# Kernel tuning notes

Measured on AMD Instinct MI355X. Metric: run time of the kernel, lower is better.

## Reference

```python
import jax, jax.numpy as jnp
import numpy as np

NC = 19
CH16, CH32 = 1024, 2048
B, H, W = 4, 64, 64
EPS = 1e-5


def bn_relu(x, gamma, beta):
    # Train-mode BatchNorm (batch statistics, as in torch default) + ReLU.
    axes = (0,) + tuple(range(2, x.ndim))  # reduce over batch + spatial
    mean = jnp.mean(x, axes, keepdims=True)
    var = jnp.var(x, axes, keepdims=True)
    shp = (1, -1) + (1,) * (x.ndim - 2)
    return jax.nn.relu((x - mean) * jax.lax.rsqrt(var + EPS) * gamma.reshape(shp) + beta.reshape(shp))


def setup_inputs() -> dict:
    key = jax.random.key(0)
    ks = jax.random.split(key, 10)
    def p(k, shape, fan):
        return jax.random.normal(k, shape, jnp.float32) / np.float32(np.sqrt(fan))
    ones = lambda c: jnp.ones((c,), jnp.float32)
    zeros = lambda c: jnp.zeros((c,), jnp.float32)
    return {
        "x": jax.random.normal(ks[0], (B, CH32, H, W), jnp.float32),
        "low_level_feature": jax.random.normal(ks[1], (B, CH16, H, W), jnp.float32),
        "W_L": p(ks[2], (NC, CH16), CH16), "b_L": zeros(NC),
        "W_X": p(ks[3], (512, CH32, 3, 3), CH32 * 9), "g_X": ones(512), "be_X": zeros(512),
        "W_phi": p(ks[4], (256, 512), 512), "g_phi": ones(256), "be_phi": zeros(256),
        "W_psi": p(ks[5], (256, 512), 512), "g_psi": ones(256), "be_psi": zeros(256),
        "W_delta": p(ks[6], (256, 512), 512), "g_delta": ones(256), "be_delta": zeros(256),
        "W_rho": p(ks[7], (512, 256), 256), "g_rho": ones(512), "be_rho": zeros(512),
        "W_g": p(ks[8], (512, 1024), 1024), "g_g": ones(512), "be_g": zeros(512),
        "W_out": p(ks[9], (NC, 512), 512), "b_out": zeros(NC),
    }


def reference(x, low_level_feature, W_L, b_L, W_X, g_X, be_X,
              W_phi, g_phi, be_phi, W_psi, g_psi, be_psi,
              W_delta, g_delta, be_delta, W_rho, g_rho, be_rho,
              W_g, g_g, be_g, W_out, b_out):
    b, _, h, w = x.shape
    # X = conv2d(2048->512, 3x3) + BN + ReLU
    Xf = jax.lax.conv_general_dilated(x, W_X, (1, 1), 'SAME',
                                      dimension_numbers=('NCHW', 'OIHW', 'NCHW'))
    Xf = bn_relu(Xf, g_X, be_X)                          # [b,512,h,w]
    # L = 1x1 conv (with bias) -> soft object regions
    L = jnp.einsum('bchw,nc->bnhw', low_level_feature, W_L) + b_L[None, :, None, None]
    l_flat = L.reshape(b, L.shape[1], -1)                # [b,nc,N]
    M = jax.nn.softmax(l_flat, axis=-1)                  # softmax over N
    X_flat = Xf.reshape(b, 512, -1)                      # [b,512,N]
    # f_k = (M @ X_flat^T)^T : object region features [b,512,nc]
    f_k = jnp.einsum('bkn,bcn->bck', M, X_flat)
    # phi/psi/delta: 1x1 conv1d + BN + ReLU
    query = bn_relu(jnp.einsum('oc,bck->bok', W_phi, f_k), g_phi, be_phi)      # [b,256,nc]
    key_ = bn_relu(jnp.einsum('oc,bcn->bon', W_psi, X_flat), g_psi, be_psi)    # [b,256,N]
    logit = jnp.einsum('bqk,bqn->bkn', query, key_)      # [b,nc,N]
    attn = jax.nn.softmax(logit, axis=1)                 # softmax over nc (dim 1)
    delta = bn_relu(jnp.einsum('oc,bck->bok', W_delta, f_k), g_delta, be_delta)  # [b,256,nc]
    attn_sum = jnp.einsum('bqk,bkn->bqn', delta, attn)   # [b,256,N]
    X_obj = bn_relu(jnp.einsum('oq,bqn->bon', W_rho, attn_sum), g_rho, be_rho)
    X_obj = X_obj.reshape(b, 512, h, w)
    concat = jnp.concatenate([Xf, X_obj], axis=1)        # [b,1024,h,w]
    X_bar = bn_relu(jnp.einsum('oc,bchw->bohw', W_g, concat), g_g, be_g)
    out = jnp.einsum('nc,bchw->bnhw', W_out, X_bar) + b_out[None, :, None, None]
    return out
```

## Files before the change

kernel.cpp:

```cpp
#include <hip/hip_runtime.h>
#include <hip/hip_bf16.h>
#include <cstdint>
#include <cstddef>

#define EPSV 1e-5f

typedef float f32x4 __attribute__((ext_vector_type(4)));
typedef _Float16 f16x8 __attribute__((ext_vector_type(8)));
typedef unsigned short ushortx8 __attribute__((ext_vector_type(8)));

__device__ __forceinline__ unsigned short f2h(float f) {
  _Float16 h = (_Float16)f;
  return *reinterpret_cast<unsigned short*>(&h);
}

__device__ __forceinline__ void gload16(const void* g, void* l) {
  __builtin_amdgcn_global_load_lds(
      (const __attribute__((address_space(1))) void*)g,
      (__attribute__((address_space(3))) void*)l, 16, 0, 0);
}

__global__ __launch_bounds__(256) void ocr_cvt_x(const float* __restrict__ x,
                                                 unsigned short* __restrict__ xT) {
  __shared__ float tile[64][65];
  int icb = blockIdx.x, h = blockIdx.y, b = blockIdx.z, t = threadIdx.x;
  const float* xp = x + ((size_t)b * 2048 + icb * 64) * 4096 + h * 64;
  #pragma unroll
  for (int r = 0; r < 16; ++r) {
    int icl = r * 4 + (t >> 6), w = t & 63;
    tile[icl][w] = xp[(size_t)icl * 4096 + w];
  }
  __syncthreads();
  #pragma unroll
  for (int it = 0; it < 2; ++it) {
    int w = it * 32 + (t >> 3), cb = (t & 7) * 8;
    ushortx8 o;
    #pragma unroll
    for (int j = 0; j < 8; ++j) o[j] = f2h(tile[cb + j][w]);
    *(ushortx8*)&xT[(((size_t)b * 66 + h + 1) * 66 + (w + 1)) * 2048 + icb * 64 + cb] = o;
  }
}

__global__ __launch_bounds__(256) void ocr_cvt_w(const float* __restrict__ Wx,
                                                 unsigned short* __restrict__ WT) {
  int oc = blockIdx.x >> 3;
  int ic = (blockIdx.x & 7) * 256 + threadIdx.x;
  const float* wp = Wx + ((size_t)oc * 2048 + ic) * 9;
  float v[9];
  #pragma unroll
  for (int t = 0; t < 9; ++t) v[t] = wp[t];
  #pragma unroll
  for (int t = 0; t < 9; ++t)
    WT[((size_t)t * 512 + oc) * 2048 + ic] = f2h(v[t]);
}

__global__ __launch_bounds__(256) void ocr_cvt_h2(const float* __restrict__ inA,
                                                  unsigned short* __restrict__ outA,
                                                  const float* __restrict__ inB,
                                                  unsigned short* __restrict__ outB) {
  int i = blockIdx.x * 256 + threadIdx.x;
  if (i < 131072) outA[i] = f2h(inA[i]);
  if (i < 524288) outB[i] = f2h(inB[i]);
}

__global__ __launch_bounds__(512, 2) void ocr_conv_mfma(const unsigned short* __restrict__ xT,
                                                        const unsigned short* __restrict__ WT,
                                                        float* __restrict__ Xf) {
  __shared__ __align__(16) char lds_raw[163840];
  float* red = (float*)lds_raw;

  const int t = threadIdx.x;
  const int wv = t >> 6, lane = t & 63;
  const int kg = lane >> 4, lc = lane & 15;
  const int ws = wv & 3, kh = wv >> 2;
  const int kh4 = kh * 4;

  const int hg  = blockIdx.x & 7;
  const int b   = (blockIdx.x >> 3) & 3;
  const int oct = blockIdx.x >> 5;
  const int oc0 = oct * 64, h0 = hg * 8;

  const char* gp[10]; int lo[10];
  #pragma unroll
  for (int i = 0; i < 10; ++i) {
    int c = wv * 10 + i;
    lo[i] = c * 1024;
    if (c < 38) {
      int cell = c * 64 + lane; if (cell > 2375) cell = 2375;
      int r = cell / 66, col = cell - r * 66; if (col > 63) col = 63;
      int tap = r >> 2, kgs = r & 3;
      gp[i] = (const char*)WT + (size_t)(((tap * 512 + oc0 + col) * 2048) + kgs * 8) * 2;
    } else {
      int c2 = c - 38;
      int cell = c2 * 64 + lane; if (cell > 2639) cell = 2639;
      int r = cell / 66, col = cell - r * 66;
      int row = r >> 2, kgs = r & 3;
      gp[i] = (const char*)xT + (size_t)((((b * 66 + h0 + row) * 66 + col) * 2048) + kgs * 8) * 2;
    }
  }

  f32x4 acc[4][8] = {};

  #pragma unroll
  for (int i = 0; i < 10; ++i) gload16(gp[i], lds_raw + lo[i]);
  asm volatile("s_waitcnt vmcnt(0)" ::: "memory");
  __builtin_amdgcn_s_barrier();

  int cur = 0;
  #pragma unroll 1
  for (int step = 0; step < 64; ++step) {
    if (step < 63) {
      unsigned adv = (unsigned)(step + 1) * 64u;
      int nxt = (cur ^ 1) * 81920;
      #pragma unroll
      for (int i = 0; i < 10; ++i) gload16(gp[i] + adv, lds_raw + nxt + lo[i]);
      asm volatile("s_waitcnt vmcnt(10)" ::: "memory");
    } else {
      asm volatile("s_waitcnt vmcnt(0)" ::: "memory");
    }
    __builtin_amdgcn_s_barrier();

    const short* As = (const short*)(lds_raw + cur * 81920);
    const short* Bs = (const short*)(lds_raw + cur * 81920 + 38912);
    __builtin_amdgcn_s_setprio(1);
    #pragma unroll
    for (int j = 0; j < 5; ++j) {
      const int tap = kh4 + j;
      const int dh = tap / 3, dw = tap - dh * 3;
      f16x8 av[4];
      #pragma unroll
      for (int mi = 0; mi < 4; ++mi)
        av[mi] = *(const f16x8*)&As[((tap * 4 + kg) * 66 + mi * 16 + lc) * 8];
      const int r0 = 2 * ws + dh;
      if ((tap != 4) || (kh == 0)) {
        #pragma unroll
        for (int nw = 0; nw < 4; ++nw) {
          f16x8 bv = *(const f16x8*)&Bs[((r0 * 4 + kg) * 66 + nw * 16 + lc + dw) * 8];
          #pragma unroll
          for (int mi = 0; mi < 4; ++mi)
            acc[mi][nw] = __builtin_amdgcn_mfma_f32_16x16x32_f16(av[mi], bv, acc[mi][nw], 0, 0, 0);
        }
      }
      if ((tap != 4) || (kh == 1)) {
        #pragma unroll
        for (int nw = 0; nw < 4; ++nw) {
          f16x8 bv = *(const f16x8*)&Bs[(((r0 + 1) * 4 + kg) * 66 + nw * 16 + lc + dw) * 8];
          #pragma unroll
          for (int mi = 0; mi < 4; ++mi)
            acc[mi][4 + nw] = __builtin_amdgcn_mfma_f32_16x16x32_f16(av[mi], bv, acc[mi][4 + nw], 0, 0, 0);
        }
      }
    }
    __builtin_amdgcn_s_setprio(0);
    asm volatile("s_waitcnt lgkmcnt(0)" ::: "memory");
    __builtin_amdgcn_sched_barrier(0);
    __builtin_amdgcn_s_barrier();
    cur ^= 1;
  }

  if (kh == 1) {
    #pragma unroll
    for (int mi = 0; mi < 4; ++mi)
      #pragma unroll
      for (int ni = 0; ni < 8; ++ni)
        *(f32x4*)&red[((ws * 32 + mi * 8 + ni) * 64 + lane) * 4] = acc[mi][ni];
  }
  __syncthreads();
  if (kh == 0) {
    #pragma unroll
    for (int mi = 0; mi < 4; ++mi) {
      #pragma unroll
      for (int ni = 0; ni < 8; ++ni) {
        f32x4 other = *(const f32x4*)&red[((ws * 32 + mi * 8 + ni) * 64 + lane) * 4];
        f32x4 s = acc[mi][ni] + other;
        int hh = ni >> 2, nw = ni & 3;
        int h = h0 + 2 * ws + hh;
        #pragma unroll
        for (int r = 0; r < 4; ++r) {
          int oc = oc0 + mi * 16 + (lane >> 4) * 4 + r;
          int w = nw * 16 + lc;
          Xf[(((size_t)b * 512 + oc) * 64 + h) * 64 + w] = s[r];
        }
      }
    }
  }
}

template<int K, int OT, int NT, int NWM, int NWN, int LDB>
__global__ __launch_bounds__(256) void ocr_gemm_h(const unsigned short* __restrict__ Ah,
                                                  const unsigned short* __restrict__ Bh,
                                                  float* __restrict__ Cm, int O) {
  static_assert(NT == 128, "NT fixed");
  constexpr int MI = OT / NWM / 16;
  constexpr int NI = NT / NWN / 16;
  constexpr int SA = OT + 2, SB = NT + 2;
  constexpr int ACELL = 4 * OT / 256;
  constexpr int ABUF = 4 * SA * 8;
  constexpr int BBUF = 4 * SB * 8;
  constexpr int NS = K / 32;
  constexpr int LPW = ACELL + 2;
  __shared__ __align__(16) short As_s[2 * ABUF];
  __shared__ __align__(16) short Bs_s[2 * BBUF];

  const int t = threadIdx.x;
  const int wv = t >> 6, lane = t & 63;
  const int kg = lane >> 4, lc = lane & 15;
  const int wm = wv / NWN, wn = wv % NWN;

  const int n0 = blockIdx.x * NT, o0 = blockIdx.y * OT, b = blockIdx.z;

  const char* aBase[ACELL]; int aLds[ACELL];
  #pragma unroll
  for (int r = 0; r < ACELL; ++r) {
    int flat0 = r * 256 + (t & 448);
    int flat  = flat0 + lane;
    int kgs = flat / OT, ol = flat % OT;
    aBase[r] = (const char*)(Ah + ((size_t)(o0 + ol)) * K + kgs * 8);
    aLds[r] = ((flat0 / OT) * SA + (flat0 % OT)) * 16;
  }
  const char* bBase[2]; int bLds[2];
  #pragma unroll
  for (int r = 0; r < 2; ++r) {
    int flat0 = r * 256 + (t & 448);
    int flat  = flat0 + lane;
    int kgs = flat >> 7, nl = flat & 127;
    bBase[r] = (const char*)(Bh + ((size_t)b * 4096 + n0 + nl) * LDB + kgs * 8);
    bLds[r] = ((flat0 >> 7) * SB + (flat0 & 127)) * 16;
  }

  f32x4 acc[MI][NI] = {};
  #pragma unroll
  for (int r = 0; r < ACELL; ++r) gload16(aBase[r], (char*)As_s + aLds[r]);
  #pragma unroll
  for (int r = 0; r < 2; ++r) gload16(bBase[r], (char*)Bs_s + bLds[r]);
  asm volatile("s_waitcnt vmcnt(0)" ::: "memory");
  __builtin_amdgcn_s_barrier();

  int cur = 0;
  #pragma unroll 1
  for (int step = 0; step < NS; ++step) {
    if (step + 1 < NS) {
      unsigned adv = (unsigned)(step + 1) * 64u;
      int nA = (cur ^ 1) * ABUF * 2, nB = (cur ^ 1) * BBUF * 2;
      #pragma unroll
      for (int r = 0; r < ACELL; ++r) gload16(aBase[r] + adv, (char*)As_s + nA + aLds[r]);
      #pragma unroll
      for (int r = 0; r < 2; ++r) gload16(bBase[r] + adv, (char*)Bs_s + nB + bLds[r]);
      if constexpr (LPW == 3) asm volatile("s_waitcnt vmcnt(3)" ::: "memory");
      else                    asm volatile("s_waitcnt vmcnt(4)" ::: "memory");
    } else {
      asm volatile("s_waitcnt vmcnt(0)" ::: "memory");
    }
    __builtin_amdgcn_s_barrier();

    const short* As = As_s + cur * ABUF;
    const short* Bsc = Bs_s + cur * BBUF;
    f16x8 av[MI], bv[NI];
    #pragma unroll
    for (int mi = 0; mi < MI; ++mi)
      av[mi] = *(const f16x8*)&As[(kg * SA + wm * (MI * 16) + mi * 16 + lc) * 8];
    #pragma unroll
    for (int ni = 0; ni < NI; ++ni)
      bv[ni] = *(const f16x8*)&Bsc[(kg * SB + wn * (NI * 16) + ni * 16 + lc) * 8];
    __builtin_amdgcn_s_setprio(1);
    #pragma unroll
    for (int mi = 0; mi < MI; ++mi)
      #pragma unroll
      for (int ni = 0; ni < NI; ++ni)
        acc[mi][ni] = __builtin_amdgcn_mfma_f32_16x16x32_f16(av[mi], bv[ni], acc[mi][ni], 0, 0, 0);
    __builtin_amdgcn_s_setprio(0);
    asm volatile("s_waitcnt lgkmcnt(0)" ::: "memory");
    __builtin_amdgcn_sched_barrier(0);
    __builtin_amdgcn_s_barrier();
    cur ^= 1;
  }
  #pragma unroll
  for (int mi = 0; mi < MI; ++mi) {
    #pragma unroll
    for (int ni = 0; ni < NI; ++ni) {
      int n = n0 + wn * (NI * 16) + ni * 16 + lc;
      #pragma unroll
      for (int r = 0; r < 4; ++r) {
        int oc = o0 + wm * (MI * 16) + mi * 16 + (lane >> 4) * 4 + r;
        Cm[((size_t)b * O + oc) * 4096 + n] = acc[mi][ni][r];
      }
    }
  }
}

__global__ __launch_bounds__(256) void ocr_t2h(const float* __restrict__ in,
                                               const float* __restrict__ scale,
                                               const float* __restrict__ shift,
                                               unsigned short* __restrict__ out,
                                               int C, int coff) {
  __shared__ float tile[64][65];
  int n0 = blockIdx.x * 64, c0 = blockIdx.y * 64, b = blockIdx.z;
  int t = threadIdx.x;
  #pragma unroll
  for (int r = 0; r < 16; ++r) {
    int c_l = r * 4 + (t >> 6), n_l = t & 63;
    tile[c_l][n_l] = in[((size_t)(b * C + c0 + c_l)) * 4096 + n0 + n_l];
  }
  __syncthreads();
  int n_l = t >> 2, cb = (t & 3) * 16;
  ushortx8 o0v, o1v;
  #pragma unroll
  for (int j = 0; j < 8; ++j) {
    int c = c0 + cb + j;
    o0v[j] = f2h(fmaxf(0.f, tile[cb + j][n_l] * scale[c] + shift[c]));
  }
  #pragma unroll
  for (int j = 0; j < 8; ++j) {
    int c = c0 + cb + 8 + j;
    o1v[j] = f2h(fmaxf(0.f, tile[cb + 8 + j][n_l] * scale[c] + shift[c]));
  }
  size_t base = ((size_t)b * 4096 + n0 + n_l) * 1024 + coff + c0 + cb;
  *(ushortx8*)&out[base] = o0v;
  *(ushortx8*)&out[base + 8] = o1v;
}

__global__ __launch_bounds__(256) void ocr_chan_stats(const float* __restrict__ buf,
                                                      const float* __restrict__ gamma,
                                                      const float* __restrict__ beta,
                                                      float* __restrict__ scale,
                                                      float* __restrict__ shift, int C) {
  int c = blockIdx.x, t = threadIdx.x;
  float s = 0.f, q = 0.f;
  for (int b = 0; b < 4; ++b) {
    const float* p = buf + ((size_t)b * C + c) * 4096;
    for (int i = t; i < 4096; i += 256) { float v = p[i]; s += v; q += v * v; }
  }
  __shared__ float ls[256], lq[256];
  ls[t] = s; lq[t] = q; __syncthreads();
  for (int off = 128; off > 0; off >>= 1) {
    if (t < off) { ls[t] += ls[t + off]; lq[t] += lq[t + off]; }
    __syncthreads();
  }
  if (t == 0) {
    float mean = ls[0] / 16384.f;
    float var  = lq[0] / 16384.f - mean * mean;
    float sc   = gamma[c] * rsqrtf(var + EPSV);
    scale[c] = sc; shift[c] = beta[c] - mean * sc;
  }
}

__global__ __launch_bounds__(256) void ocr_lproj(const float* __restrict__ llf,
                                                 const float* __restrict__ WL,
                                                 const float* __restrict__ bL,
                                                 float* __restrict__ L) {
  int h = blockIdx.x, b = blockIdx.y;
  int t = threadIdx.x, w = t & 63, csub = t >> 6;
  float acc[19];
  #pragma unroll
  for (int k = 0; k < 19; ++k) acc[k] = 0.f;
  const float* base = llf + ((size_t)b * 1024 + csub * 256) * 4096 + h * 64 + w;
  #pragma unroll 1
  for (int c4 = 0; c4 < 64; ++c4) {
    float lv[4];
    #pragma unroll
    for (int i = 0; i < 4; ++i) lv[i] = base[(size_t)(c4 + i * 64) * 4096];
    #pragma unroll
    for (int i = 0; i < 4; ++i) {
      const float* wl = &WL[csub * 256 + c4 + i * 64];
      #pragma unroll
      for (int k = 0; k < 19; ++k) acc[k] += wl[k * 1024] * lv[i];
    }
  }
  __shared__ float red[4][64][19];
  #pragma unroll
  for (int k = 0; k < 19; ++k) red[csub][w][k] = acc[k];
  __syncthreads();
  if (csub == 0) {
    #pragma unroll
    for (int k = 0; k < 19; ++k) {
      float s = red[0][w][k] + red[1][w][k] + red[2][w][k] + red[3][w][k] + bL[k];
      L[((size_t)b * 19 + k) * 4096 + h * 64 + w] = s;
    }
  }
}

__global__ __launch_bounds__(256) void ocr_softmax4096(float* __restrict__ buf) {
  int row = blockIdx.x, t = threadIdx.x;
  float* p = buf + (size_t)row * 4096;
  __shared__ float ls[256];
  float m = -1e30f;
  for (int i = t; i < 4096; i += 256) m = fmaxf(m, p[i]);
  ls[t] = m; __syncthreads();
  for (int off = 128; off > 0; off >>= 1) { if (t < off) ls[t] = fmaxf(ls[t], ls[t + off]); __syncthreads(); }
  m = ls[0]; __syncthreads();
  float s = 0.f;
  for (int i = t; i < 4096; i += 256) { float e = __expf(p[i] - m); p[i] = e; s += e; }
  ls[t] = s; __syncthreads();
  for (int off = 128; off > 0; off >>= 1) { if (t < off) ls[t] += ls[t + off]; __syncthreads(); }
  float inv = 1.f / ls[0];
  for (int i = t; i < 4096; i += 256) p[i] *= inv;
}

__global__ __launch_bounds__(256) void ocr_fk(const float* __restrict__ M,
                                              const float* __restrict__ Xf,
                                              const float* __restrict__ scale,
                                              const float* __restrict__ shift,
                                              float* __restrict__ fk) {
  int c = blockIdx.x, b = blockIdx.y, t = threadIdx.x;
  float acc[19];
  #pragma unroll
  for (int k = 0; k < 19; ++k) acc[k] = 0.f;
  const float* xp = Xf + ((size_t)b * 512 + c) * 4096;
  const float* mp = M + (size_t)b * 19 * 4096;
  float sc = scale[c], sh = shift[c];
  for (int n = t; n < 4096; n += 256) {
    float xv = fmaxf(0.f, xp[n] * sc + sh);
    #pragma unroll
    for (int k = 0; k < 19; ++k) acc[k] += mp[k * 4096 + n] * xv;
  }
  __shared__ float red[19 * 256];
  #pragma unroll
  for (int k = 0; k < 19; ++k) red[k * 256 + t] = acc[k];
  __syncthreads();
  for (int off = 128; off > 0; off >>= 1) {
    if (t < off) {
      #pragma unroll
      for (int k = 0; k < 19; ++k) red[k * 256 + t] += red[k * 256 + t + off];
    }
    __syncthreads();
  }
  if (t < 19) fk[((size_t)b * 512 + c) * 19 + t] = red[t * 256];
}

__global__ __launch_bounds__(256) void ocr_qd2(const float* __restrict__ Wphi,
                                               const float* __restrict__ Wdelta,
                                               const float* __restrict__ fk,
                                               float* __restrict__ qry,
                                               float* __restrict__ dlt) {
  int blk = blockIdx.x;
  const float* Wm = (blk < 76) ? Wphi : Wdelta;
  float* out = (blk < 76) ? qry : dlt;
  int tid = (blk < 76 ? blk : blk - 76) * 256 + threadIdx.x;
  if (tid >= 4 * 256 * 19) return;
  int k = tid % 19, o = (tid / 19) % 256, b = tid / (19 * 256);
  const float* fp = fk + (size_t)b * 512 * 19 + k;
  const float* wp = Wm + (size_t)o * 512;
  float acc = 0.f;
  for (int c = 0; c < 512; ++c) acc += wp[c] * fp[c * 19];
  out[tid] = acc;
}

__global__ __launch_bounds__(128) void ocr_bn76x2(float* __restrict__ qry,
                                                  float* __restrict__ dlt,
                                                  const float* __restrict__ g_phi,
                                                  const float* __restrict__ be_phi,
                                                  const float* __restrict__ g_delta,
                                                  const float* __restrict__ be_delta) {
  bool second = blockIdx.x >= 256;
  int o = blockIdx.x & 255, t = threadIdx.x;
  float* buf = second ? dlt : qry;
  const float* gamma = second ? g_delta : g_phi;
  const float* beta  = second ? be_delta : be_phi;
  bool act = t < 76;
  float v = 0.f;
  size_t idx = 0;
  if (act) {
    int b = t / 19, k = t % 19;
    idx = ((size_t)b * 256 + o) * 19 + k;
    v = buf[idx];
  }
  __shared__ float ls[128], lq[128];
  ls[t] = act ? v : 0.f; lq[t] = act ? v * v : 0.f; __syncthreads();
  for (int off = 64; off > 0; off >>= 1) { if (t < off) { ls[t] += ls[t + off]; lq[t] += lq[t + off]; } __syncthreads(); }
  __shared__ float s_sc, s_sh;
  if (t == 0) {
    float mean = ls[0] / 76.f;
    float var  = lq[0] / 76.f - mean * mean;
    float sc   = gamma[o] * rsqrtf(var + EPSV);
    s_sc = sc; s_sh = beta[o] - mean * sc;
  }
  __syncthreads();
  if (act) buf[idx] = fmaxf(0.f, v * s_sc + s_sh);
}

__global__ __launch_bounds__(256) void ocr_attn(const float* __restrict__ query,
                                                const float* __restrict__ key,
                                                const float* __restrict__ scale,
                                                const float* __restrict__ shift,
                                                float* __restrict__ attn) {
  int n0 = blockIdx.x * 64, b = blockIdx.y;
  int t = threadIdx.x, nl = t & 63, qsub = t >> 6;
  __shared__ float ql[256 * 19];
  for (int i = t; i < 256 * 19; i += 256) ql[i] = query[(size_t)b * 256 * 19 + i];
  __syncthreads();
  float acc[19];
  #pragma unroll
  for (int k = 0; k < 19; ++k) acc[k] = 0.f;
  const float* kp = key + ((size_t)b * 256 + qsub * 64) * 4096 + n0 + nl;
  #pragma unroll 1
  for (int q4 = 0; q4 < 64; q4 += 4) {
    float kv[4];
    #pragma unroll
    for (int i = 0; i < 4; ++i) kv[i] = kp[(size_t)(q4 + i) * 4096];
    #pragma unroll
    for (int i = 0; i < 4; ++i) {
      int ch = qsub * 64 + q4 + i;
      float kva = fmaxf(0.f, kv[i] * scale[ch] + shift[ch]);
      const float* qq = &ql[ch * 19];
      #pragma unroll
      for (int k = 0; k < 19; ++k) acc[k] += qq[k] * kva;
    }
  }
  __shared__ float red[4][64][19];
  #pragma unroll
  for (int k = 0; k < 19; ++k) red[qsub][nl][k] = acc[k];
  __syncthreads();
  if (qsub == 0) {
    float v[19]; float m = -1e30f;
    #pragma unroll
    for (int k = 0; k < 19; ++k) {
      v[k] = red[0][nl][k] + red[1][nl][k] + red[2][nl][k] + red[3][nl][k];
      m = fmaxf(m, v[k]);
    }
    float s = 0.f;
    #pragma unroll
    for (int k = 0; k < 19; ++k) { v[k] = __expf(v[k] - m); s += v[k]; }
    float inv = 1.f / s;
    #pragma unroll
    for (int k = 0; k < 19; ++k)
      attn[((size_t)b * 19 + k) * 4096 + n0 + nl] = v[k] * inv;
  }
}

__global__ __launch_bounds__(256) void ocr_wd(const float* __restrict__ Wrho,
                                              const float* __restrict__ dlt,
                                              float* __restrict__ Wd) {
  int tid = blockIdx.x * 256 + threadIdx.x;
  if (tid >= 4 * 512 * 19) return;
  int k = tid % 19, o = (tid / 19) % 512, b = tid / (19 * 512);
  const float* dp = dlt + (size_t)b * 256 * 19 + k;
  const float* wp = Wrho + (size_t)o * 256;
  float acc = 0.f;
  for (int q = 0; q < 256; ++q) acc += wp[q] * dp[q * 19];
  Wd[tid] = acc;
}

__global__ __launch_bounds__(256) void ocr_xobj_stats(const float* __restrict__ Wd,
                                                      const float* __restrict__ attn,
                                                      const float* __restrict__ gamma,
                                                      const float* __restrict__ beta,
                                                      float* __restrict__ scale,
                                                      float* __restrict__ shift) {
  int o = blockIdx.x, t = threadIdx.x;
  float s = 0.f, q = 0.f;
  for (int b = 0; b < 4; ++b) {
    float wd[19];
    #pragma unroll
    for (int k = 0; k < 19; ++k) wd[k] = Wd[((size_t)b * 512 + o) * 19 + k];
    for (int n = t; n < 4096; n += 256) {
      float v = 0.f;
      #pragma unroll
      for (int k = 0; k < 19; ++k) v += wd[k] * attn[((size_t)b * 19 + k) * 4096 + n];
      s += v; q += v * v;
    }
  }
  __shared__ float ls[256], lq[256];
  ls[t] = s; lq[t] = q; __syncthreads();
  for (int off = 128; off > 0; off >>= 1) {
    if (t < off) { ls[t] += ls[t + off]; lq[t] += lq[t + off]; }
    __syncthreads();
  }
  if (t == 0) {
    float mean = ls[0] / 16384.f;
    float var  = lq[0] / 16384.f - mean * mean;
    float sc   = gamma[o] * rsqrtf(var + EPSV);
    scale[o] = sc; shift[o] = beta[o] - mean * sc;
  }
}

__global__ __launch_bounds__(512) void ocr_xobj_apply(const float* __restrict__ Wd,
                                                      const float* __restrict__ attn,
                                                      const float* __restrict__ scale,
                                                      const float* __restrict__ shift,
                                                      unsigned short* __restrict__ ch) {
  __shared__ float al[19][256];
  int n0 = blockIdx.x * 256, b = blockIdx.y, o = threadIdx.x;
  for (int idx = o; idx < 19 * 256; idx += 512) {
    int k = idx >> 8, nl = idx & 255;
    al[k][nl] = attn[((size_t)b * 19 + k) * 4096 + n0 + nl];
  }
  float wd[19];
  #pragma unroll
  for (int k = 0; k < 19; ++k) wd[k] = Wd[((size_t)b * 512 + o) * 19 + k];
  float sc = scale[o], sh = shift[o];
  __syncthreads();
  #pragma unroll 1
  for (int nl = 0; nl < 256; ++nl) {
    float v = 0.f;
    #pragma unroll
    for (int k = 0; k < 19; ++k) v += wd[k] * al[k][nl];
    v = fmaxf(0.f, v * sc + sh);
    ch[((size_t)b * 4096 + n0 + nl) * 1024 + 512 + o] = f2h(v);
  }
}

__global__ __launch_bounds__(256) void ocr_out(const float* __restrict__ Wout,
                                               const float* __restrict__ bout,
                                               const float* __restrict__ Xbar,
                                               const float* __restrict__ scale,
                                               const float* __restrict__ shift,
                                               float* __restrict__ out) {
  int n0 = blockIdx.x * 64, b = blockIdx.y;
  int t = threadIdx.x, nl = t & 63, csub = t >> 6;
  float acc[19];
  #pragma unroll
  for (int k = 0; k < 19; ++k) acc[k] = 0.f;
  const float* base = Xbar + ((size_t)b * 512 + csub * 128) * 4096 + n0 + nl;
  #pragma unroll 1
  for (int c4 = 0; c4 < 128; c4 += 4) {
    float xv[4];
    #pragma unroll
    for (int i = 0; i < 4; ++i) xv[i] = base[(size_t)(c4 + i) * 4096];
    #pragma unroll
    for (int i = 0; i < 4; ++i) {
      int chn = csub * 128 + c4 + i;
      float a = fmaxf(0.f, xv[i] * scale[chn] + shift[chn]);
      #pragma unroll
      for (int k = 0; k < 19; ++k) acc[k] += Wout[k * 512 + chn] * a;
    }
  }
  __shared__ float red[4][64][19];
  #pragma unroll
  for (int k = 0; k < 19; ++k) red[csub][nl][k] = acc[k];
  __syncthreads();
  if (csub == 0) {
    #pragma unroll
    for (int k = 0; k < 19; ++k) {
      float s = red[0][nl][k] + red[1][nl][k] + red[2][nl][k] + red[3][nl][k] + bout[k];
      out[((size_t)b * 19 + k) * 4096 + n0 + nl] = s;
    }
  }
}

extern "C" void kernel_launch(void* const* d_in, const int* in_sizes, int n_in,
                              void* d_out, int out_size, void* d_ws, size_t ws_size,
                              hipStream_t stream) {
  const float* x    = (const float*)d_in[0];
  const float* llf  = (const float*)d_in[1];
  const float* W_L  = (const float*)d_in[2];
  const float* b_L  = (const float*)d_in[3];
  const float* W_X  = (const float*)d_in[4];
  const float* g_X  = (const float*)d_in[5];
  const float* be_X = (const float*)d_in[6];
  const float* W_phi = (const float*)d_in[7];
  const float* g_phi = (const float*)d_in[8];
  const float* be_phi = (const float*)d_in[9];
  const float* W_psi = (const float*)d_in[10];
  const float* g_psi = (const float*)d_in[11];
  const float* be_psi = (const float*)d_in[12];
  const float* W_delta = (const float*)d_in[13];
  const float* g_delta = (const float*)d_in[14];
  const float* be_delta = (const float*)d_in[15];
  const float* W_rho = (const float*)d_in[16];
  const float* g_rho = (const float*)d_in[17];
  const float* be_rho = (const float*)d_in[18];
  const float* W_g  = (const float*)d_in[19];
  const float* g_g  = (const float*)d_in[20];
  const float* be_g = (const float*)d_in[21];
  const float* W_out = (const float*)d_in[22];
  const float* b_out = (const float*)d_in[23];

  float* ws = (float*)d_ws;
  float* Xf = ws;
  float* U  = ws + 8388608;
  unsigned short* xT = (unsigned short*)U;
  unsigned short* WT = (unsigned short*)(U + 17842176);
  unsigned short* concat_h = (unsigned short*)U;
  float* key  = U + 8388608;
  float* Xbar = U + 12582912;
  float* SM   = U + 22560768;
  float* M     = SM;
  float* attnb = SM + 311296;
  float* fk    = SM + 622592;
  float* qry   = SM + 661504;
  float* dlt   = SM + 680960;
  float* Wd    = SM + 700416;
  float* st    = SM + 739328;
  unsigned short* Wpsi_h = (unsigned short*)(SM + 743424);
  unsigned short* Wg_h   = (unsigned short*)(SM + 808960);
  float* scX = st,        *shX = st + 512;
  float* scP = st + 1024, *shP = st + 1280;
  float* scR = st + 1536, *shR = st + 2048;
  float* scG = st + 2560, *shG = st + 3072;

  hipMemsetAsync(xT, 0, (size_t)35684352 * sizeof(unsigned short), stream);
  ocr_cvt_x<<<dim3(32, 64, 4), 256, 0, stream>>>(x, xT);
  ocr_cvt_w<<<dim3(4096), 256, 0, stream>>>(W_X, WT);
  ocr_cvt_h2<<<dim3(2048), 256, 0, stream>>>(W_psi, Wpsi_h, W_g, Wg_h);

  ocr_conv_mfma<<<dim3(256), 512, 0, stream>>>(xT, WT, Xf);

  ocr_chan_stats<<<dim3(512), 256, 0, stream>>>(Xf, g_X, be_X, scX, shX, 512);
  ocr_t2h<<<dim3(64, 8, 4), 256, 0, stream>>>(Xf, scX, shX, concat_h, 512, 0);
  ocr_lproj<<<dim3(64, 4), 256, 0, stream>>>(llf, W_L, b_L, M);
  ocr_softmax4096<<<dim3(76), 256, 0, stream>>>(M);
  ocr_fk<<<dim3(512, 4), 256, 0, stream>>>(M, Xf, scX, shX, fk);
  ocr_qd2<<<dim3(152), 256, 0, stream>>>(W_phi, W_delta, fk, qry, dlt);
  ocr_bn76x2<<<dim3(512), 128, 0, stream>>>(qry, dlt, g_phi, be_phi, g_delta, be_delta);
  ocr_gemm_h<512, 64, 128, 2, 2, 1024><<<dim3(32, 4, 4), 256, 0, stream>>>(Wpsi_h, concat_h, key, 256);
  ocr_chan_stats<<<dim3(256), 256, 0, stream>>>(key, g_psi, be_psi, scP, shP, 256);
  ocr_attn<<<dim3(64, 4), 256, 0, stream>>>(qry, key, scP, shP, attnb);
  ocr_wd<<<dim3(152), 256, 0, stream>>>(W_rho, dlt, Wd);
  ocr_xobj_stats<<<dim3(512), 256, 0, stream>>>(Wd, attnb, g_rho, be_rho, scR, shR);
  ocr_xobj_apply<<<dim3(16, 4), 512, 0, stream>>>(Wd, attnb, scR, shR, concat_h);
  ocr_gemm_h<1024, 128, 128, 2, 2, 1024><<<dim3(32, 4, 4), 256, 0, stream>>>(Wg_h, concat_h, Xbar, 512);
  ocr_chan_stats<<<dim3(512), 256, 0, stream>>>(Xbar, g_g, be_g, scG, shG, 512);
  ocr_out<<<dim3(64, 4), 256, 0, stream>>>(W_out, b_out, Xbar, scG, shG, (float*)d_out);
}
```

Before: 822.9 us.

## Double conv block to 1024 threads with one output row per wave

Grows the 3x3 conv MFMA kernel from 8 to 16 waves per block. Each wave now computes a single output row, so its accumulator set is halved and it issues half as many global-to-LDS loads. The centre tap is split across the two K-halves by output column halves instead of by row. The hand-tuned vmcnt waits, priority hints and scheduling barriers are replaced with plain __syncthreads, which costs fine-grained load/compute overlap. The launch-bounds hint of (1024, 4) may force a tight register budget and cause spills.

```diff
diff --git a/kernel.cpp b/kernel.cpp
--- a/kernel.cpp
+++ b/kernel.cpp
@@ -63,27 +63,26 @@
   if (i < 524288) outB[i] = f2h(inB[i]);
 }
 
-__global__ __launch_bounds__(512, 2) void ocr_conv_mfma(const unsigned short* __restrict__ xT,
-                                                        const unsigned short* __restrict__ WT,
-                                                        float* __restrict__ Xf) {
+__global__ __launch_bounds__(1024, 4) void ocr_conv_mfma(const unsigned short* __restrict__ xT,
+                                                         const unsigned short* __restrict__ WT,
+                                                         float* __restrict__ Xf) {
   __shared__ __align__(16) char lds_raw[163840];
   float* red = (float*)lds_raw;
 
   const int t = threadIdx.x;
   const int wv = t >> 6, lane = t & 63;
   const int kg = lane >> 4, lc = lane & 15;
-  const int ws = wv & 3, kh = wv >> 2;
-  const int kh4 = kh * 4;
+  const int ws = wv & 7, kh = wv >> 3;
 
   const int hg  = blockIdx.x & 7;
   const int b   = (blockIdx.x >> 3) & 3;
   const int oct = blockIdx.x >> 5;
   const int oc0 = oct * 64, h0 = hg * 8;
 
-  const char* gp[10]; int lo[10];
-  #pragma unroll
-  for (int i = 0; i < 10; ++i) {
-    int c = wv * 10 + i;
+  const char* gp[5]; int lo[5];
+  #pragma unroll
+  for (int i = 0; i < 5; ++i) {
+    int c = wv * 5 + i;
     lo[i] = c * 1024;
     if (c < 38) {
       int cell = c * 64 + lane; if (cell > 2375) cell = 2375;
@@ -99,12 +98,11 @@
     }
   }
 
-  f32x4 acc[4][8] = {};
-
-  #pragma unroll
-  for (int i = 0; i < 10; ++i) gload16(gp[i], lds_raw + lo[i]);
-  asm volatile("s_waitcnt vmcnt(0)" ::: "memory");
-  __builtin_amdgcn_s_barrier();
+  f32x4 acc[4][4] = {};
+
+  #pragma unroll
+  for (int i = 0; i < 5; ++i) gload16(gp[i], lds_raw + lo[i]);
+  __syncthreads();
 
   int cur = 0;
   #pragma unroll 1
@@ -113,48 +111,32 @@
       unsigned adv = (unsigned)(step + 1) * 64u;
       int nxt = (cur ^ 1) * 81920;
       #pragma unroll
-      for (int i = 0; i < 10; ++i) gload16(gp[i] + adv, lds_raw + nxt + lo[i]);
-      asm volatile("s_waitcnt vmcnt(10)" ::: "memory");
-    } else {
-      asm volatile("s_waitcnt vmcnt(0)" ::: "memory");
-    }
-    __builtin_amdgcn_s_barrier();
-
+      for (int i = 0; i < 5; ++i) gload16(gp[i] + adv, lds_raw + nxt + lo[i]);
+    }
     const short* As = (const short*)(lds_raw + cur * 81920);
     const short* Bs = (const short*)(lds_raw + cur * 81920 + 38912);
-    __builtin_amdgcn_s_setprio(1);
     #pragma unroll
     for (int j = 0; j < 5; ++j) {
-      const int tap = kh4 + j;
+      const int tap = kh * 4 + j;
       const int dh = tap / 3, dw = tap - dh * 3;
       f16x8 av[4];
       #pragma unroll
       for (int mi = 0; mi < 4; ++mi)
         av[mi] = *(const f16x8*)&As[((tap * 4 + kg) * 66 + mi * 16 + lc) * 8];
-      const int r0 = 2 * ws + dh;
-      if ((tap != 4) || (kh == 0)) {
-        #pragma unroll
-        for (int nw = 0; nw < 4; ++nw) {
-          f16x8 bv = *(const f16x8*)&Bs[((r0 * 4 + kg) * 66 + nw * 16 + lc + dw) * 8];
+      const int row = ws + dh;
+      const int nw0 = (tap == 4) ? (kh ? 2 : 0) : 0;
+      const int nwN = (tap == 4) ? (nw0 + 2) : 4;
+      #pragma unroll
+      for (int nw = 0; nw < 4; ++nw) {
+        if (nw >= nw0 && nw < nwN) {
+          f16x8 bv = *(const f16x8*)&Bs[((row * 4 + kg) * 66 + nw * 16 + lc + dw) * 8];
           #pragma unroll
           for (int mi = 0; mi < 4; ++mi)
             acc[mi][nw] = __builtin_amdgcn_mfma_f32_16x16x32_f16(av[mi], bv, acc[mi][nw], 0, 0, 0);
         }
       }
-      if ((tap != 4) || (kh == 1)) {
-        #pragma unroll
-        for (int nw = 0; nw < 4; ++nw) {
-          f16x8 bv = *(const f16x8*)&Bs[(((r0 + 1) * 4 + kg) * 66 + nw * 16 + lc + dw) * 8];
-          #pragma unroll
-          for (int mi = 0; mi < 4; ++mi)
-            acc[mi][4 + nw] = __builtin_amdgcn_mfma_f32_16x16x32_f16(av[mi], bv, acc[mi][4 + nw], 0, 0, 0);
-        }
-      }
-    }
-    __builtin_amdgcn_s_setprio(0);
-    asm volatile("s_waitcnt lgkmcnt(0)" ::: "memory");
-    __builtin_amdgcn_sched_barrier(0);
-    __builtin_amdgcn_s_barrier();
+    }
+    __syncthreads();
     cur ^= 1;
   }
 
@@ -162,19 +144,18 @@
     #pragma unroll
     for (int mi = 0; mi < 4; ++mi)
       #pragma unroll
-      for (int ni = 0; ni < 8; ++ni)
-        *(f32x4*)&red[((ws * 32 + mi * 8 + ni) * 64 + lane) * 4] = acc[mi][ni];
+      for (int nw = 0; nw < 4; ++nw)
+        *(f32x4*)&red[(((ws * 16 + mi * 4 + nw) * 64) + lane) * 4] = acc[mi][nw];
   }
   __syncthreads();
   if (kh == 0) {
+    const int h = h0 + ws;
     #pragma unroll
     for (int mi = 0; mi < 4; ++mi) {
       #pragma unroll
-      for (int ni = 0; ni < 8; ++ni) {
-        f32x4 other = *(const f32x4*)&red[((ws * 32 + mi * 8 + ni) * 64 + lane) * 4];
-        f32x4 s = acc[mi][ni] + other;
-        int hh = ni >> 2, nw = ni & 3;
-        int h = h0 + 2 * ws + hh;
+      for (int nw = 0; nw < 4; ++nw) {
+        f32x4 other = *(const f32x4*)&red[(((ws * 16 + mi * 4 + nw) * 64) + lane) * 4];
+        f32x4 s = acc[mi][nw] + other;
         #pragma unroll
         for (int r = 0; r < 4; ++r) {
           int oc = oc0 + mi * 16 + (lane >> 4) * 4 + r;
@@ -693,7 +674,7 @@
   ocr_cvt_w<<<dim3(4096), 256, 0, stream>>>(W_X, WT);
   ocr_cvt_h2<<<dim3(2048), 256, 0, stream>>>(W_psi, Wpsi_h, W_g, Wg_h);
 
-  ocr_conv_mfma<<<dim3(256), 512, 0, stream>>>(xT, WT, Xf);
+  ocr_conv_mfma<<<dim3(256), 1024, 0, stream>>>(xT, WT, Xf);
 
   ocr_chan_stats<<<dim3(512), 256, 0, stream>>>(Xf, g_X, be_X, scX, shX, 512);
   ocr_t2h<<<dim3(64, 8, 4), 256, 0, stream>>>(Xf, scX, shX, concat_h, 512, 0);
```

Result: faster. 748.6 us (-9.0%).
